# Optimization experiments

Measured on AMD Instinct MI355X. Metric: run time of the kernel, lower is better.

## Reference

```python
import jax, jax.numpy as jnp
import numpy as np

N_P, E_P = 150000, 1200000   # protein nodes / edges (512 complexes batched)
N_L, E_L = 16000, 64000      # ligand nodes / edges
E_I = 400000                 # interaction (distance) edges, bidirectional
B, D, L = 512, 64, 3         # graphs, hidden_dim_g, num_g_layers
ND, ED = 58, 6               # initial node / edge feature dims


def edge_softmax(logits, dst, n):
    # softmax over incoming edges of each destination node
    m = jax.ops.segment_max(logits, dst, num_segments=n)
    ex = jnp.exp(logits - m[dst])
    s = jax.ops.segment_sum(ex, dst, num_segments=n)
    return ex / (s[dst] + 1e-9)


def gcn_layer(h, src, dst, W, n):
    # GraphConvolution: sum-aggregate neighbors, linear, relu, residual
    agg = jax.ops.segment_sum(h[src], dst, num_segments=n)
    return jax.nn.relu(agg @ W) + h


def gat_layer(h, e, src, dst, Wh, We, a_s, a_d, a_e, n):
    # GraphAttention (edge-feature aware GAT): additive attention logits,
    # edge-softmax by destination, weighted message sum, relu, residual.
    x = h @ Wh                      # [N, D]
    ee = e @ We                     # [E, D]
    logit = jax.nn.leaky_relu(
        (x[src] * a_s).sum(-1) + (x[dst] * a_d).sum(-1) + (ee * a_e).sum(-1), 0.2)
    alpha = edge_softmax(logit, dst, n)
    out = jax.ops.segment_sum(alpha[:, None] * (x[src] + ee), dst, num_segments=n)
    return jax.nn.relu(out) + h


def setup_inputs() -> dict:
    key = jax.random.key(0)
    ks = jax.random.split(key, 40)
    p = lambda k, shape: jax.random.normal(k, shape, jnp.float32) * 0.05
    h_p = jax.random.normal(ks[0], (N_P, ND), jnp.float32)
    e_p = jax.random.normal(ks[1], (E_P, ED), jnp.float32)
    src_p = jax.random.randint(ks[2], (E_P,), 0, N_P, jnp.int32)
    dst_p = jax.random.randint(ks[3], (E_P,), 0, N_P, jnp.int32)
    h_l = jax.random.normal(ks[4], (N_L, ND), jnp.float32)
    e_l = jax.random.normal(ks[5], (E_L, ED), jnp.float32)
    src_l = jax.random.randint(ks[6], (E_L,), 0, N_L, jnp.int32)
    dst_l = jax.random.randint(ks[7], (E_L,), 0, N_L, jnp.int32)
    coordinate = jax.random.normal(ks[8], (N_P + N_L, 3), jnp.float32) * 10.0
    # interaction edges: protein <-> ligand (ligand nodes offset by N_P)
    sp = jax.random.randint(ks[9], (E_I // 2,), 0, N_P, jnp.int32)
    dl = jax.random.randint(ks[10], (E_I // 2,), N_P, N_P + N_L, jnp.int32)
    src_i = jnp.concatenate([sp, dl])
    dst_i = jnp.concatenate([dl, sp])
    # graph ids for batched readout (balanced partition, monotone)
    gid_p = jnp.asarray(np.arange(N_P) * B // N_P, jnp.int32)
    gid_l = jnp.asarray(np.arange(N_L) * B // N_L, jnp.int32)
    gid_j = jnp.concatenate([gid_p, gid_l])
    return {
        'h_p': h_p, 'e_p': e_p, 'src_p': src_p, 'dst_p': dst_p,
        'h_l': h_l, 'e_l': e_l, 'src_l': src_l, 'dst_l': dst_l,
        'coordinate': coordinate, 'src_i': src_i, 'dst_i': dst_i, 'gid_j': gid_j,
        'Wn_p': p(ks[11], (ND, D)), 'We_p': p(ks[12], (ED, D)),
        'Wn_l': p(ks[13], (ND, D)), 'We_l': p(ks[14], (ED, D)),
        'Wemb_in': p(ks[15], (D, D)), 'Wemb_ie': p(ks[16], (1, D)),
        'Wc': p(ks[17], (L, D, D)),
        'Al_h': p(ks[18], (L, D, D)), 'Al_e': p(ks[19], (L, D, D)),
        'al_s': p(ks[20], (L, D)), 'al_d': p(ks[21], (L, D)), 'al_e': p(ks[22], (L, D)),
        'Ai_h': p(ks[23], (L, D, D)), 'Ai_e': p(ks[24], (L, D, D)),
        'ai_s': p(ks[25], (L, D)), 'ai_d': p(ks[26], (L, D)), 'ai_e': p(ks[27], (L, D)),
        'W1': p(ks[28], (D, D)), 'W2': p(ks[29], (D, 1)),
    }


def reference(h_p, e_p, src_p, dst_p, h_l, e_l, src_l, dst_l, coordinate,
              src_i, dst_i, gid_j, Wn_p, We_p, Wn_l, We_l, Wemb_in, Wemb_ie,
              Wc, Al_h, Al_e, al_s, al_d, al_e, Ai_h, Ai_e, ai_s, ai_d, ai_e,
              W1, W2):
    # node / edge embeddings (bias-free linears)
    hp = h_p @ Wn_p
    ep = e_p @ We_p
    hl = h_l @ Wn_l
    el = e_l @ We_l
    n_p, n_l = hp.shape[0], hl.shape[0]
    # protein branch: GraphConvolution stack
    for i in range(Wc.shape[0]):
        hp = gcn_layer(hp, src_p, dst_p, Wc[i], n_p)
    # ligand branch: GraphAttention stack (bond edge features)
    for i in range(Al_h.shape[0]):
        hl = gat_layer(hl, el, src_l, dst_l, Al_h[i], Al_e[i],
                       al_s[i], al_d[i], al_e[i], n_l)
    # join graphs: node states concatenated, edge feature = pair distance
    hj = jnp.concatenate([hp, hl], axis=0) @ Wemb_in          # [N_P+N_L, D]
    dist = jnp.sqrt(((coordinate[src_i] - coordinate[dst_i]) ** 2)
                    .sum(-1, keepdims=True) + 1e-12)           # [E_I, 1]
    vdw = dist @ Wemb_ie                                       # [E_I, D]
    n_j = n_p + n_l
    for i in range(Ai_h.shape[0]):
        hj = gat_layer(hj, vdw, src_i, dst_i, Ai_h[i], Ai_e[i],
                       ai_s[i], ai_d[i], ai_e[i], n_j)
    # sum readout per complex, then 2-layer bias-free MLP
    readout = jax.ops.segment_sum(hj, gid_j, num_segments=B)   # [B, D]
    return jax.nn.relu(readout @ W1) @ W2                      # [B, 1]
```

## Files before the change

kernel.cpp:

```cpp
#include <hip/hip_runtime.h>
#include <math.h>

#define THREADS 256

#define N_P 150000
#define E_P 1200000
#define N_L 16000
#define E_L 64000
#define E_I 400000
#define N_J (N_P + N_L)
#define NB  512
#define DIM 64
#define NLAYER 3
#define SCAN_TILE 1024

typedef float f4 __attribute__((ext_vector_type(4)));

static __device__ __forceinline__ float wred_sum(float v) {
    #pragma unroll
    for (int o = 32; o; o >>= 1) v += __shfl_xor(v, o);
    return v;
}
static __device__ __forceinline__ float gred_max(float v) {
    #pragma unroll
    for (int o = 1; o <= 8; o <<= 1) v = fmaxf(v, __shfl_xor(v, o));
    return v;
}
static __device__ __forceinline__ float gred_sum(float v) {
    #pragma unroll
    for (int o = 1; o <= 8; o <<= 1) v += __shfl_xor(v, o);
    return v;
}

__global__ void hist_k(const int* __restrict__ dst, int* __restrict__ cnt,
                       int* __restrict__ slot, int E)
{
    int e = blockIdx.x * THREADS + threadIdx.x;
    if (e >= E) return;
    slot[e] = atomicAdd(&cnt[dst[e]], 1);
}

__global__ void scan_local(const int* __restrict__ in, int* __restrict__ out,
                           int* __restrict__ partials, int n)
{
    __shared__ int lds[256];
    int t = threadIdx.x;
    int base = blockIdx.x * SCAN_TILE + t * 4;
    int v0 = base + 0 < n ? in[base + 0] : 0;
    int v1 = base + 1 < n ? in[base + 1] : 0;
    int v2 = base + 2 < n ? in[base + 2] : 0;
    int v3 = base + 3 < n ? in[base + 3] : 0;
    int s = v0 + v1 + v2 + v3;
    lds[t] = s;
    __syncthreads();
    #pragma unroll
    for (int off = 1; off < 256; off <<= 1) {
        int x = (t >= off) ? lds[t - off] : 0;
        __syncthreads();
        lds[t] += x;
        __syncthreads();
    }
    int excl = lds[t] - s;
    if (base + 0 < n) out[base + 0] = excl;
    if (base + 1 < n) out[base + 1] = excl + v0;
    if (base + 2 < n) out[base + 2] = excl + v0 + v1;
    if (base + 3 < n) out[base + 3] = excl + v0 + v1 + v2;
    if (t == 255) partials[blockIdx.x] = lds[255];
}

__global__ void scan_part(int* __restrict__ partials, int np)
{
    __shared__ int lds[256];
    int t = threadIdx.x;
    int v = t < np ? partials[t] : 0;
    lds[t] = v;
    __syncthreads();
    #pragma unroll
    for (int off = 1; off < 256; off <<= 1) {
        int x = (t >= off) ? lds[t - off] : 0;
        __syncthreads();
        lds[t] += x;
        __syncthreads();
    }
    if (t < np) partials[t] = lds[t] - v;
}

__global__ void scan_add(int* __restrict__ out, const int* __restrict__ partials,
                         int n, int etotal)
{
    int i = blockIdx.x * THREADS + threadIdx.x;
    if (i < n) out[i] += partials[i / SCAN_TILE];
    if (i == 0) out[n] = etotal;
}

__global__ void fill_p_k(const int* __restrict__ src, const int* __restrict__ dst,
                         const int* __restrict__ slot, const int* __restrict__ rp,
                         int* __restrict__ esrc, int E)
{
    int e = blockIdx.x * THREADS + threadIdx.x;
    if (e >= E) return;
    esrc[rp[dst[e]] + slot[e]] = src[e];
}

__global__ void fill_l_k(const int* __restrict__ src, const int* __restrict__ dst,
                         const int* __restrict__ slot, const int* __restrict__ rp,
                         int* __restrict__ esrc, int* __restrict__ eid, int E)
{
    int e = blockIdx.x * THREADS + threadIdx.x;
    if (e >= E) return;
    int pos = rp[dst[e]] + slot[e];
    esrc[pos] = src[e];
    eid[pos] = e;
}

__global__ void fill_i_k(const int* __restrict__ src, const int* __restrict__ dst,
                         const int* __restrict__ slot, const int* __restrict__ rp,
                         const float* __restrict__ coord,
                         int* __restrict__ esrc, float* __restrict__ dsorted, int E)
{
    int e = blockIdx.x * THREADS + threadIdx.x;
    if (e >= E) return;
    int s = src[e], d = dst[e];
    int pos = rp[d] + slot[e];
    esrc[pos] = s;
    float dx = coord[s * 3 + 0] - coord[d * 3 + 0];
    float dy = coord[s * 3 + 1] - coord[d * 3 + 1];
    float dz = coord[s * 3 + 2] - coord[d * 3 + 2];
    dsorted[pos] = sqrtf(dx * dx + dy * dy + dz * dz + 1e-12f);
}

template<int K, int EPI>
__global__ __launch_bounds__(256, 8)
void gemm64_k(const float* __restrict__ X, const float* __restrict__ W,
              const float* __restrict__ RES, const float* __restrict__ a1,
              const float* __restrict__ a2, float* __restrict__ Y,
              float* __restrict__ S1, float* __restrict__ S2, int N)
{
    __shared__ float Xs[64][68];
    int t = threadIdx.x;
    int tx = t & 15, ty = t >> 4;
    int rbase = blockIdx.x * 64;
    if constexpr (K % 4 == 0) {
        #pragma unroll
        for (int j = t; j < 16 * K; j += 256) {
            int r = j / (K / 4), k4 = j % (K / 4);
            int row = rbase + r;
            f4 v = {0.f, 0.f, 0.f, 0.f};
            if (row < N) v = *(const f4*)&X[(long)row * K + k4 * 4];
            *(f4*)&Xs[r][k4 * 4] = v;
        }
    } else {
        for (int j = t; j < 64 * K; j += 256) {
            int r = j / K, k = j - r * K;
            int row = rbase + r;
            Xs[r][k] = (row < N) ? X[(long)row * K + k] : 0.f;
        }
    }
    __syncthreads();
    f4 acc[4] = {{0,0,0,0},{0,0,0,0},{0,0,0,0},{0,0,0,0}};
    #pragma unroll 4
    for (int k = 0; k < K; ++k) {
        f4 wv = *(const f4*)&W[k * DIM + tx * 4];
        #pragma unroll
        for (int i = 0; i < 4; ++i) {
            float xv = Xs[ty * 4 + i][k];
            acc[i] += wv * xv;
        }
    }
    #pragma unroll
    for (int i = 0; i < 4; ++i) {
        int row = rbase + ty * 4 + i;
        if (row >= N) continue;
        f4 y = acc[i];
        if constexpr (EPI == 1) {
            f4 res = *(const f4*)&RES[(long)row * DIM + tx * 4];
            #pragma unroll
            for (int c = 0; c < 4; ++c) y[c] = fmaxf(y[c], 0.f) + res[c];
        }
        *(f4*)&Y[(long)row * DIM + tx * 4] = y;
    }
    if constexpr (EPI == 2) {
        f4 a1v = *(const f4*)&a1[tx * 4];
        f4 a2v = *(const f4*)&a2[tx * 4];
        #pragma unroll
        for (int i = 0; i < 4; ++i) {
            float s = acc[i][0]*a1v[0] + acc[i][1]*a1v[1] + acc[i][2]*a1v[2] + acc[i][3]*a1v[3];
            float d = acc[i][0]*a2v[0] + acc[i][1]*a2v[1] + acc[i][2]*a2v[2] + acc[i][3]*a2v[3];
            #pragma unroll
            for (int o = 1; o <= 8; o <<= 1) {
                s += __shfl_xor(s, o);
                d += __shfl_xor(d, o);
            }
            int row = rbase + ty * 4 + i;
            if (tx == 0 && row < N) { S1[row] = s; S2[row] = d; }
        }
    }
    if constexpr (EPI == 3) {
        f4 a1v = *(const f4*)&a1[tx * 4];
        #pragma unroll
        for (int i = 0; i < 4; ++i) {
            float s = acc[i][0]*a1v[0] + acc[i][1]*a1v[1] + acc[i][2]*a1v[2] + acc[i][3]*a1v[3];
            #pragma unroll
            for (int o = 1; o <= 8; o <<= 1) s += __shfl_xor(s, o);
            int row = rbase + ty * 4 + i;
            if (tx == 0 && row < N) S1[row] = s;
        }
    }
}

template<int JOIN>
__global__ __launch_bounds__(256, 6)
void gcn_fused_k(const float* __restrict__ Hin, const int* __restrict__ rp,
                 const int* __restrict__ esrc, const float* __restrict__ W,
                 const float* __restrict__ W2, float* __restrict__ Hout, int N)
{
    __shared__ float Xs[32][68];
    __shared__ float Ws[64][64];
    int t = threadIdx.x;
    int gl = t & 15, g = t >> 4, wb = (t & 63) & 48;
    int rbase = blockIdx.x * 32;
    for (int i = t; i < 1024; i += 256)
        *(f4*)&Ws[(i * 4) >> 6][(i * 4) & 63] = *(const f4*)&W[i * 4];
    #pragma unroll
    for (int it = 0; it < 2; ++it) {
        int ln = it * 16 + g;
        int node = rbase + ln;
        f4 acc = {0.f, 0.f, 0.f, 0.f};
        if (node < N) {
            int lo = rp[node], hi = rp[node + 1];
            for (int cb = lo; cb < hi; cb += 16) {
                int cnt = min(16, hi - cb);
                int sidx = (gl < cnt) ? esrc[cb + gl] : 0;
                int p = 0;
                for (; p + 3 < cnt; p += 4) {
                    int s0 = __shfl(sidx, wb + p + 0);
                    int s1 = __shfl(sidx, wb + p + 1);
                    int s2 = __shfl(sidx, wb + p + 2);
                    int s3 = __shfl(sidx, wb + p + 3);
                    f4 v0 = *(const f4*)&Hin[(long)s0 * DIM + gl * 4];
                    f4 v1 = *(const f4*)&Hin[(long)s1 * DIM + gl * 4];
                    f4 v2 = *(const f4*)&Hin[(long)s2 * DIM + gl * 4];
                    f4 v3 = *(const f4*)&Hin[(long)s3 * DIM + gl * 4];
                    acc += v0; acc += v1; acc += v2; acc += v3;
                }
                for (; p < cnt; ++p) {
                    int s = __shfl(sidx, wb + p);
                    acc += *(const f4*)&Hin[(long)s * DIM + gl * 4];
                }
            }
        }
        *(f4*)&Xs[ln][gl * 4] = acc;
    }
    __syncthreads();
    int tx = t & 15, ty = t >> 4;
    f4 acc[2] = {{0,0,0,0},{0,0,0,0}};
    #pragma unroll 4
    for (int k = 0; k < DIM; ++k) {
        f4 wv = *(const f4*)&Ws[k][tx * 4];
        acc[0] += wv * Xs[ty * 2 + 0][k];
        acc[1] += wv * Xs[ty * 2 + 1][k];
    }
    f4 yv[2];
    #pragma unroll
    for (int i = 0; i < 2; ++i) {
        int row = rbase + ty * 2 + i;
        int rr = row < N ? row : 0;
        f4 res = *(const f4*)&Hin[(long)rr * DIM + tx * 4];
        #pragma unroll
        for (int c = 0; c < 4; ++c) yv[i][c] = fmaxf(acc[i][c], 0.f) + res[c];
    }
    if constexpr (!JOIN) {
        #pragma unroll
        for (int i = 0; i < 2; ++i) {
            int row = rbase + ty * 2 + i;
            if (row < N) *(f4*)&Hout[(long)row * DIM + tx * 4] = yv[i];
        }
    } else {
        __syncthreads();
        *(f4*)&Xs[ty * 2 + 0][tx * 4] = yv[0];
        *(f4*)&Xs[ty * 2 + 1][tx * 4] = yv[1];
        for (int i = t; i < 1024; i += 256)
            *(f4*)&Ws[(i * 4) >> 6][(i * 4) & 63] = *(const f4*)&W2[i * 4];
        __syncthreads();
        f4 a2[2] = {{0,0,0,0},{0,0,0,0}};
        #pragma unroll 4
        for (int k = 0; k < DIM; ++k) {
            f4 wv = *(const f4*)&Ws[k][tx * 4];
            a2[0] += wv * Xs[ty * 2 + 0][k];
            a2[1] += wv * Xs[ty * 2 + 1][k];
        }
        #pragma unroll
        for (int i = 0; i < 2; ++i) {
            int row = rbase + ty * 2 + i;
            if (row < N) *(f4*)&Hout[(long)row * DIM + tx * 4] = a2[i];
        }
    }
}

__global__ __launch_bounds__(256, 8)
void gat_l_k(const float* __restrict__ X, const float* __restrict__ Sn,
             const float* __restrict__ Dn, const float* __restrict__ Et,
             const float* __restrict__ EE, const int* __restrict__ rp,
             const int* __restrict__ esrc, const int* __restrict__ eid,
             float* __restrict__ H, int N)
{
    int t = threadIdx.x;
    int gl = t & 15, g = t >> 4, wb = (t & 63) & 48;
    int node = blockIdx.x * 16 + g;
    int lo = 0, hi = 0;
    float dn = 0.f;
    if (node < N) { lo = rp[node]; hi = rp[node + 1]; dn = Dn[node]; }
    float m = -INFINITY, ssum = 0.f;
    f4 msg = {0.f, 0.f, 0.f, 0.f};
    for (int cb = lo; cb < hi; cb += 16) {
        int cnt = min(16, hi - cb);
        int sidx = 0, eidx = 0;
        float l = -INFINITY;
        if (gl < cnt) {
            sidx = esrc[cb + gl];
            eidx = eid[cb + gl];
            l = Sn[sidx] + dn + Et[eidx];
            l = (l >= 0.f) ? l : 0.2f * l;
        }
        float mnew = fmaxf(m, gred_max(l));
        float scale = expf(m - mnew);
        float ex = (gl < cnt) ? expf(l - mnew) : 0.f;
        ssum = ssum * scale + gred_sum(ex);
        msg *= scale;
        int p = 0;
        for (; p + 1 < cnt; p += 2) {
            float e0 = __shfl(ex, wb + p + 0); int s0 = __shfl(sidx, wb + p + 0);
            int   q0 = __shfl(eidx, wb + p + 0);
            float e1 = __shfl(ex, wb + p + 1); int s1 = __shfl(sidx, wb + p + 1);
            int   q1 = __shfl(eidx, wb + p + 1);
            f4 x0 = *(const f4*)&X[(long)s0 * DIM + gl * 4];
            f4 f0 = *(const f4*)&EE[(long)q0 * DIM + gl * 4];
            f4 x1 = *(const f4*)&X[(long)s1 * DIM + gl * 4];
            f4 f1 = *(const f4*)&EE[(long)q1 * DIM + gl * 4];
            msg += (x0 + f0) * e0;
            msg += (x1 + f1) * e1;
        }
        for (; p < cnt; ++p) {
            float ep = __shfl(ex, wb + p);
            int s = __shfl(sidx, wb + p);
            int e = __shfl(eidx, wb + p);
            f4 xv = *(const f4*)&X[(long)s * DIM + gl * 4];
            f4 ev = *(const f4*)&EE[(long)e * DIM + gl * 4];
            msg += (xv + ev) * ep;
        }
        m = mnew;
    }
    float inv = 1.f / (ssum + 1e-9f);
    if (node < N) {
        long o = (long)node * DIM + gl * 4;
        f4 h = *(const f4*)&H[o];
        f4 r;
        #pragma unroll
        for (int c = 0; c < 4; ++c) r[c] = fmaxf(msg[c] * inv, 0.f) + h[c];
        *(f4*)&H[o] = r;
    }
}

__global__ __launch_bounds__(256, 8)
void gat_i_k(const float* __restrict__ X, const float* __restrict__ Sn,
             const float* __restrict__ Dn, const float* __restrict__ dsorted,
             const float* __restrict__ cbuf, const int* __restrict__ rp,
             const int* __restrict__ esrc, float* __restrict__ H, int N)
{
    int t = threadIdx.x;
    int gl = t & 15, g = t >> 4, wb = (t & 63) & 48;
    int node = blockIdx.x * 16 + g;
    float ce = cbuf[64];
    int lo = 0, hi = 0;
    float dn = 0.f;
    if (node < N) { lo = rp[node]; hi = rp[node + 1]; dn = Dn[node]; }
    float m = -INFINITY, ssum = 0.f, wl = 0.f;
    f4 msg = {0.f, 0.f, 0.f, 0.f};
    for (int cb = lo; cb < hi; cb += 16) {
        int cnt = min(16, hi - cb);
        int sidx = 0;
        float dv = 0.f, l = -INFINITY;
        if (gl < cnt) {
            sidx = esrc[cb + gl];
            dv = dsorted[cb + gl];
            l = Sn[sidx] + dn + dv * ce;
            l = (l >= 0.f) ? l : 0.2f * l;
        }
        float mnew = fmaxf(m, gred_max(l));
        float scale = expf(m - mnew);
        float ex = (gl < cnt) ? expf(l - mnew) : 0.f;
        ssum = ssum * scale + gred_sum(ex);
        wl = wl * scale + ex * dv;
        msg *= scale;
        int p = 0;
        for (; p + 3 < cnt; p += 4) {
            float e0 = __shfl(ex, wb + p + 0); int s0 = __shfl(sidx, wb + p + 0);
            float e1 = __shfl(ex, wb + p + 1); int s1 = __shfl(sidx, wb + p + 1);
            float e2 = __shfl(ex, wb + p + 2); int s2 = __shfl(sidx, wb + p + 2);
            float e3 = __shfl(ex, wb + p + 3); int s3 = __shfl(sidx, wb + p + 3);
            f4 v0 = *(const f4*)&X[(long)s0 * DIM + gl * 4];
            f4 v1 = *(const f4*)&X[(long)s1 * DIM + gl * 4];
            f4 v2 = *(const f4*)&X[(long)s2 * DIM + gl * 4];
            f4 v3 = *(const f4*)&X[(long)s3 * DIM + gl * 4];
            msg += v0 * e0; msg += v1 * e1; msg += v2 * e2; msg += v3 * e3;
        }
        for (; p < cnt; ++p) {
            float ep = __shfl(ex, wb + p);
            int s = __shfl(sidx, wb + p);
            msg += *(const f4*)&X[(long)s * DIM + gl * 4] * ep;
        }
        m = mnew;
    }
    float wsum = gred_sum(wl);
    float inv = 1.f / (ssum + 1e-9f);
    if (node < N) {
        long o = (long)node * DIM + gl * 4;
        f4 c4 = *(const f4*)&cbuf[gl * 4];
        f4 h = *(const f4*)&H[o];
        f4 r;
        #pragma unroll
        for (int c = 0; c < 4; ++c) {
            float v = (msg[c] + wsum * c4[c]) * inv;
            r[c] = fmaxf(v, 0.f) + h[c];
        }
        *(f4*)&H[o] = r;
    }
}

__global__ void cvec_all_k(const float* __restrict__ wie, const float* __restrict__ Ae,
                           const float* __restrict__ ae, float* __restrict__ cbuf)
{
    int L = blockIdx.x;
    int d = threadIdx.x;
    const float* A = Ae + (size_t)L * DIM * DIM;
    float c = 0.f;
    #pragma unroll
    for (int k = 0; k < DIM; ++k) c = fmaf(wie[k], A[k * DIM + d], c);
    cbuf[L * 80 + d] = c;
    float ce = wred_sum(c * ae[L * DIM + d]);
    if (d == 0) cbuf[L * 80 + 64] = ce;
}

__global__ __launch_bounds__(256, 1)
void readout_mlp_k(const float* __restrict__ HJ, const float* __restrict__ W1,
                   const float* __restrict__ W2, float* __restrict__ out)
{
    __shared__ float part[4][DIM];
    int t = threadIdx.x, wv = t >> 6, lane = t & 63;
    int b = blockIdx.x;
    float r = 0.f;
    long s0 = ((long)b * N_P + NB - 1) / NB;
    long e0 = ((long)(b + 1) * N_P + NB - 1) / NB;
    for (long n = s0 + wv; n < e0; n += 4) r += HJ[n * DIM + lane];
    long s1 = ((long)b * N_L + NB - 1) / NB;
    long e1 = ((long)(b + 1) * N_L + NB - 1) / NB;
    for (long n = s1 + wv; n < e1; n += 4) r += HJ[(N_P + n) * DIM + lane];
    part[wv][lane] = r;
    __syncthreads();
    if (wv != 0) return;
    r = part[0][lane] + part[1][lane] + part[2][lane] + part[3][lane];
    float acc = 0.f;
    #pragma unroll
    for (int k = 0; k < DIM; ++k) acc = fmaf(__shfl(r, k), W1[k * DIM + lane], acc);
    acc = fmaxf(acc, 0.f) * W2[lane];
    acc = wred_sum(acc);
    if (lane == 0) out[b] = acc;
}

extern "C" void kernel_launch(void* const* d_in, const int* in_sizes, int n_in,
                              void* d_out, int out_size, void* d_ws, size_t ws_size,
                              hipStream_t stream) {
    const float* h_p    = (const float*)d_in[0];
    const int*   src_p  = (const int*)d_in[2];
    const int*   dst_p  = (const int*)d_in[3];
    const float* h_l    = (const float*)d_in[4];
    const float* e_l    = (const float*)d_in[5];
    const int*   src_l  = (const int*)d_in[6];
    const int*   dst_l  = (const int*)d_in[7];
    const float* coord  = (const float*)d_in[8];
    const int*   src_i  = (const int*)d_in[9];
    const int*   dst_i  = (const int*)d_in[10];
    const float* Wn_p   = (const float*)d_in[12];
    const float* Wn_l   = (const float*)d_in[14];
    const float* We_l   = (const float*)d_in[15];
    const float* Wemb_in= (const float*)d_in[16];
    const float* Wemb_ie= (const float*)d_in[17];
    const float* Wc     = (const float*)d_in[18];
    const float* Al_h   = (const float*)d_in[19];
    const float* Al_e   = (const float*)d_in[20];
    const float* al_s   = (const float*)d_in[21];
    const float* al_d   = (const float*)d_in[22];
    const float* al_e   = (const float*)d_in[23];
    const float* Ai_h   = (const float*)d_in[24];
    const float* Ai_e   = (const float*)d_in[25];
    const float* ai_s   = (const float*)d_in[26];
    const float* ai_d   = (const float*)d_in[27];
    const float* ai_e   = (const float*)d_in[28];
    const float* W1     = (const float*)d_in[29];
    const float* W2     = (const float*)d_in[30];
    float* out = (float*)d_out;

    char* ws = (char*)d_ws;
    auto alloc = [&](size_t bytes) -> void* {
        char* p = ws;
        ws += (bytes + 255) & ~(size_t)255;
        return (void*)p;
    };
    float* HP    = (float*)alloc((size_t)N_P * DIM * 4);
    float* HL    = (float*)alloc((size_t)N_L * DIM * 4);
    float* EL    = (float*)alloc((size_t)E_L * DIM * 4);
    float* EE    = (float*)alloc((size_t)E_L * DIM * 4);
    float* HJ    = (float*)alloc((size_t)N_J * DIM * 4);
    float* XJ    = (float*)alloc((size_t)N_J * DIM * 4);
    float* SN    = (float*)alloc((size_t)N_J * 4);
    float* DN    = (float*)alloc((size_t)N_J * 4);
    float* ET    = (float*)alloc((size_t)E_L * 4);
    int*   cnt_p = (int*)alloc((size_t)N_P * 4);
    int*   cnt_l = (int*)alloc((size_t)N_L * 4);
    int*   cnt_i = (int*)alloc((size_t)N_J * 4);
    int*   rp_p  = (int*)alloc((size_t)(N_P + 1) * 4);
    int*   rp_l  = (int*)alloc((size_t)(N_L + 1) * 4);
    int*   rp_i  = (int*)alloc((size_t)(N_J + 1) * 4);
    int*   slot  = (int*)alloc((size_t)E_P * 4);
    int*   esrc_p= (int*)alloc((size_t)E_P * 4);
    int*   esrc_l= (int*)alloc((size_t)E_L * 4);
    int*   eid_l = (int*)alloc((size_t)E_L * 4);
    int*   esrc_i= (int*)alloc((size_t)E_I * 4);
    float* dsort = (float*)alloc((size_t)E_I * 4);
    int*   parts = (int*)alloc(256 * 4);
    float* CBUF  = (float*)alloc(3 * 80 * 4);
    (void)ws_size; (void)in_sizes; (void)n_in; (void)out_size;

    auto cdiv = [](int a, int b) { return (a + b - 1) / b; };

    hipMemsetAsync(cnt_p, 0, (size_t)N_P * 4, stream);
    hipMemsetAsync(cnt_l, 0, (size_t)N_L * 4, stream);
    hipMemsetAsync(cnt_i, 0, (size_t)N_J * 4, stream);
    auto build = [&](const int* dst, int* cnt, int* rp, int E, int N) {
        hist_k<<<cdiv(E, THREADS), THREADS, 0, stream>>>(dst, cnt, slot, E);
        int nb = cdiv(N, SCAN_TILE);
        scan_local<<<nb, 256, 0, stream>>>(cnt, rp, parts, N);
        scan_part<<<1, 256, 0, stream>>>(parts, nb);
        scan_add<<<cdiv(N, THREADS), THREADS, 0, stream>>>(rp, parts, N, E);
    };
    build(dst_p, cnt_p, rp_p, E_P, N_P);
    fill_p_k<<<cdiv(E_P, THREADS), THREADS, 0, stream>>>(src_p, dst_p, slot, rp_p, esrc_p, E_P);
    build(dst_l, cnt_l, rp_l, E_L, N_L);
    fill_l_k<<<cdiv(E_L, THREADS), THREADS, 0, stream>>>(src_l, dst_l, slot, rp_l, esrc_l, eid_l, E_L);
    build(dst_i, cnt_i, rp_i, E_I, N_J);
    fill_i_k<<<cdiv(E_I, THREADS), THREADS, 0, stream>>>(src_i, dst_i, slot, rp_i, coord, esrc_i, dsort, E_I);

    cvec_all_k<<<3, 64, 0, stream>>>(Wemb_ie, Ai_e, ai_e, CBUF);

    gemm64_k<58, 0><<<cdiv(N_P, 64), THREADS, 0, stream>>>(h_p, Wn_p, nullptr, nullptr, nullptr,
                                                           HP, nullptr, nullptr, N_P);
    gemm64_k<58, 0><<<cdiv(N_L, 64), THREADS, 0, stream>>>(h_l, Wn_l, nullptr, nullptr, nullptr,
                                                           HL, nullptr, nullptr, N_L);
    gemm64_k<6, 0><<<cdiv(E_L, 64), THREADS, 0, stream>>>(e_l, We_l, nullptr, nullptr, nullptr,
                                                          EL, nullptr, nullptr, E_L);

    for (int i = 0; i < NLAYER; ++i) {
        const float* Wh = Al_h + (size_t)i * DIM * DIM;
        const float* We = Al_e + (size_t)i * DIM * DIM;
        gemm64_k<64, 2><<<cdiv(N_L, 64), THREADS, 0, stream>>>(HL, Wh, nullptr,
                                                               al_s + i * DIM, al_d + i * DIM,
                                                               XJ, SN, DN, N_L);
        gemm64_k<64, 3><<<cdiv(E_L, 64), THREADS, 0, stream>>>(EL, We, nullptr,
                                                               al_e + i * DIM, nullptr,
                                                               EE, ET, nullptr, E_L);
        gat_l_k<<<cdiv(N_L, 16), THREADS, 0, stream>>>(XJ, SN, DN, ET, EE, rp_l, esrc_l,
                                                       eid_l, HL, N_L);
    }

    gcn_fused_k<0><<<cdiv(N_P, 32), THREADS, 0, stream>>>(HP, rp_p, esrc_p,
                                                          Wc + 0 * DIM * DIM, nullptr, XJ, N_P);
    gcn_fused_k<0><<<cdiv(N_P, 32), THREADS, 0, stream>>>(XJ, rp_p, esrc_p,
                                                          Wc + 1 * (size_t)DIM * DIM, nullptr, HP, N_P);
    gcn_fused_k<1><<<cdiv(N_P, 32), THREADS, 0, stream>>>(HP, rp_p, esrc_p,
                                                          Wc + 2 * (size_t)DIM * DIM, Wemb_in, HJ, N_P);

    gemm64_k<64, 0><<<cdiv(N_L, 64), THREADS, 0, stream>>>(HL, Wemb_in, nullptr, nullptr, nullptr,
                                                           HJ + (size_t)N_P * DIM, nullptr, nullptr, N_L);

    for (int i = 0; i < NLAYER; ++i) {
        const float* Wh = Ai_h + (size_t)i * DIM * DIM;
        gemm64_k<64, 2><<<cdiv(N_J, 64), THREADS, 0, stream>>>(HJ, Wh, nullptr,
                                                               ai_s + i * DIM, ai_d + i * DIM,
                                                               XJ, SN, DN, N_J);
        gat_i_k<<<cdiv(N_J, 16), THREADS, 0, stream>>>(XJ, SN, DN, dsort, CBUF + i * 80, rp_i,
                                                       esrc_i, HJ, N_J);
    }

    readout_mlp_k<<<NB, THREADS, 0, stream>>>(HJ, W1, W2, out);
}
```

Baseline: 742.2 us.

## Fuse interaction GAT projection into aggregation via aggregate-then-transform reordering

Each interaction GAT layer used to run a separate GEMM producing X = H·Wh plus attention scalars, then a gather kernel over X. Attention scalars are now computed from H directly using precomputed Wh·a_s and Wh·a_d vectors, H is aggregated with softmax weights, and the aggregate is multiplied by Wh inside the same kernel. The next layer's scalars come from the epilogue, and the GCN and ligand embedding kernels emit the first layer's scalars. This drops three GEMM launches and their N×64 intermediate round trips, at the cost of ping-pong buffers and lower occupancy in the fused kernel.

Result: faster. 688.6 us (-7.2%).

```diff
diff --git a/kernel.cpp b/kernel.cpp
--- a/kernel.cpp
+++ b/kernel.cpp
@@ -31,6 +31,12 @@
     for (int o = 1; o <= 8; o <<= 1) v += __shfl_xor(v, o);
     return v;
 }
+static __device__ __forceinline__ float gdot16(f4 y, f4 a) {
+    float s = y[0]*a[0] + y[1]*a[1] + y[2]*a[2] + y[3]*a[3];
+    #pragma unroll
+    for (int o = 1; o <= 8; o <<= 1) s += __shfl_xor(s, o);
+    return s;
+}
 
 __global__ void hist_k(const int* __restrict__ dst, int* __restrict__ cnt,
                        int* __restrict__ slot, int E)
@@ -212,7 +218,9 @@
 __global__ __launch_bounds__(256, 6)
 void gcn_fused_k(const float* __restrict__ Hin, const int* __restrict__ rp,
                  const int* __restrict__ esrc, const float* __restrict__ W,
-                 const float* __restrict__ W2, float* __restrict__ Hout, int N)
+                 const float* __restrict__ W2, const float* __restrict__ ash,
+                 const float* __restrict__ adh, float* __restrict__ Hout,
+                 float* __restrict__ SnO, float* __restrict__ DnO, int N)
 {
     __shared__ float Xs[32][68];
     __shared__ float Ws[64][64];
@@ -294,6 +302,126 @@
             int row = rbase + ty * 2 + i;
             if (row < N) *(f4*)&Hout[(long)row * DIM + tx * 4] = a2[i];
         }
+        f4 av = *(const f4*)&ash[tx * 4];
+        f4 bv = *(const f4*)&adh[tx * 4];
+        float s0 = gdot16(a2[0], av);
+        float d0 = gdot16(a2[0], bv);
+        float s1 = gdot16(a2[1], av);
+        float d1 = gdot16(a2[1], bv);
+        if (tx == 0) {
+            int row0 = rbase + ty * 2, row1 = row0 + 1;
+            if (row0 < N) { SnO[row0] = s0; DnO[row0] = d0; }
+            if (row1 < N) { SnO[row1] = s1; DnO[row1] = d1; }
+        }
+    }
+}
+
+template<int LAST>
+__global__ __launch_bounds__(256, 6)
+void gat_i_fused_k(const float* __restrict__ Hin, const float* __restrict__ Sn,
+                   const float* __restrict__ Dn, const float* __restrict__ dsorted,
+                   const float* __restrict__ pb, const float* __restrict__ pbn,
+                   const float* __restrict__ Wh, const int* __restrict__ rp,
+                   const int* __restrict__ esrc, float* __restrict__ Hout,
+                   float* __restrict__ SnO, float* __restrict__ DnO, int N)
+{
+    __shared__ float Xs[32][68];
+    __shared__ float Ws[64][64];
+    __shared__ float wlS[32];
+    __shared__ float invS[32];
+    int t = threadIdx.x;
+    int gl = t & 15, g = t >> 4, wb = (t & 63) & 48;
+    int rbase = blockIdx.x * 32;
+    float ce = pb[64];
+    for (int i = t; i < 1024; i += 256)
+        *(f4*)&Ws[(i * 4) >> 6][(i * 4) & 63] = *(const f4*)&Wh[i * 4];
+    #pragma unroll
+    for (int it = 0; it < 2; ++it) {
+        int ln = it * 16 + g;
+        int node = rbase + ln;
+        int lo = 0, hi = 0;
+        float dn = 0.f;
+        if (node < N) { lo = rp[node]; hi = rp[node + 1]; dn = Dn[node]; }
+        float m = -INFINITY, ssum = 0.f, wl = 0.f;
+        f4 agg = {0.f, 0.f, 0.f, 0.f};
+        for (int cb = lo; cb < hi; cb += 16) {
+            int cnt = min(16, hi - cb);
+            int sidx = 0;
+            float dv = 0.f, l = -INFINITY;
+            if (gl < cnt) {
+                sidx = esrc[cb + gl];
+                dv = dsorted[cb + gl];
+                l = Sn[sidx] + dn + dv * ce;
+                l = (l >= 0.f) ? l : 0.2f * l;
+            }
+            float mnew = fmaxf(m, gred_max(l));
+            float scale = expf(m - mnew);
+            float ex = (gl < cnt) ? expf(l - mnew) : 0.f;
+            ssum = ssum * scale + gred_sum(ex);
+            wl = wl * scale + ex * dv;
+            agg *= scale;
+            int p = 0;
+            for (; p + 3 < cnt; p += 4) {
+                float e0 = __shfl(ex, wb + p + 0); int s0 = __shfl(sidx, wb + p + 0);
+                float e1 = __shfl(ex, wb + p + 1); int s1 = __shfl(sidx, wb + p + 1);
+                float e2 = __shfl(ex, wb + p + 2); int s2 = __shfl(sidx, wb + p + 2);
+                float e3 = __shfl(ex, wb + p + 3); int s3 = __shfl(sidx, wb + p + 3);
+                f4 v0 = *(const f4*)&Hin[(long)s0 * DIM + gl * 4];
+                f4 v1 = *(const f4*)&Hin[(long)s1 * DIM + gl * 4];
+                f4 v2 = *(const f4*)&Hin[(long)s2 * DIM + gl * 4];
+                f4 v3 = *(const f4*)&Hin[(long)s3 * DIM + gl * 4];
+                agg += v0 * e0; agg += v1 * e1; agg += v2 * e2; agg += v3 * e3;
+            }
+            for (; p < cnt; ++p) {
+                float ep = __shfl(ex, wb + p);
+                int s = __shfl(sidx, wb + p);
+                agg += *(const f4*)&Hin[(long)s * DIM + gl * 4] * ep;
+            }
+            m = mnew;
+        }
+        float wsum = gred_sum(wl);
+        *(f4*)&Xs[ln][gl * 4] = agg;
+        if (gl == 0) {
+            wlS[ln] = wsum;
+            invS[ln] = 1.f / (ssum + 1e-9f);
+        }
+    }
+    __syncthreads();
+    int tx = t & 15, ty = t >> 4;
+    f4 acc0 = {0,0,0,0}, acc1 = {0,0,0,0};
+    #pragma unroll 4
+    for (int k = 0; k < DIM; ++k) {
+        f4 wv = *(const f4*)&Ws[k][tx * 4];
+        acc0 += wv * Xs[ty * 2 + 0][k];
+        acc1 += wv * Xs[ty * 2 + 1][k];
+    }
+    int r0 = ty * 2, r1 = r0 + 1;
+    int row0 = rbase + r0, row1 = rbase + r1;
+    f4 c4 = *(const f4*)&pb[tx * 4];
+    float wl0 = wlS[r0], wl1 = wlS[r1];
+    float i0 = invS[r0], i1 = invS[r1];
+    int rr0 = row0 < N ? row0 : 0, rr1 = row1 < N ? row1 : 0;
+    f4 h0 = *(const f4*)&Hin[(long)rr0 * DIM + tx * 4];
+    f4 h1 = *(const f4*)&Hin[(long)rr1 * DIM + tx * 4];
+    f4 y0, y1;
+    #pragma unroll
+    for (int c = 0; c < 4; ++c) {
+        y0[c] = fmaxf((acc0[c] + wl0 * c4[c]) * i0, 0.f) + h0[c];
+        y1[c] = fmaxf((acc1[c] + wl1 * c4[c]) * i1, 0.f) + h1[c];
+    }
+    if (row0 < N) *(f4*)&Hout[(long)row0 * DIM + tx * 4] = y0;
+    if (row1 < N) *(f4*)&Hout[(long)row1 * DIM + tx * 4] = y1;
+    if constexpr (!LAST) {
+        f4 av = *(const f4*)&pbn[80 + tx * 4];
+        f4 bv = *(const f4*)&pbn[144 + tx * 4];
+        float s0 = gdot16(y0, av);
+        float d0 = gdot16(y0, bv);
+        float s1 = gdot16(y1, av);
+        float d1 = gdot16(y1, bv);
+        if (tx == 0) {
+            if (row0 < N) { SnO[row0] = s0; DnO[row0] = d0; }
+            if (row1 < N) { SnO[row1] = s1; DnO[row1] = d1; }
+        }
     }
 }
 
@@ -361,84 +489,30 @@
     }
 }
 
-__global__ __launch_bounds__(256, 8)
-void gat_i_k(const float* __restrict__ X, const float* __restrict__ Sn,
-             const float* __restrict__ Dn, const float* __restrict__ dsorted,
-             const float* __restrict__ cbuf, const int* __restrict__ rp,
-             const int* __restrict__ esrc, float* __restrict__ H, int N)
-{
-    int t = threadIdx.x;
-    int gl = t & 15, g = t >> 4, wb = (t & 63) & 48;
-    int node = blockIdx.x * 16 + g;
-    float ce = cbuf[64];
-    int lo = 0, hi = 0;
-    float dn = 0.f;
-    if (node < N) { lo = rp[node]; hi = rp[node + 1]; dn = Dn[node]; }
-    float m = -INFINITY, ssum = 0.f, wl = 0.f;
-    f4 msg = {0.f, 0.f, 0.f, 0.f};
-    for (int cb = lo; cb < hi; cb += 16) {
-        int cnt = min(16, hi - cb);
-        int sidx = 0;
-        float dv = 0.f, l = -INFINITY;
-        if (gl < cnt) {
-            sidx = esrc[cb + gl];
-            dv = dsorted[cb + gl];
-            l = Sn[sidx] + dn + dv * ce;
-            l = (l >= 0.f) ? l : 0.2f * l;
-        }
-        float mnew = fmaxf(m, gred_max(l));
-        float scale = expf(m - mnew);
-        float ex = (gl < cnt) ? expf(l - mnew) : 0.f;
-        ssum = ssum * scale + gred_sum(ex);
-        wl = wl * scale + ex * dv;
-        msg *= scale;
-        int p = 0;
-        for (; p + 3 < cnt; p += 4) {
-            float e0 = __shfl(ex, wb + p + 0); int s0 = __shfl(sidx, wb + p + 0);
-            float e1 = __shfl(ex, wb + p + 1); int s1 = __shfl(sidx, wb + p + 1);
-            float e2 = __shfl(ex, wb + p + 2); int s2 = __shfl(sidx, wb + p + 2);
-            float e3 = __shfl(ex, wb + p + 3); int s3 = __shfl(sidx, wb + p + 3);
-            f4 v0 = *(const f4*)&X[(long)s0 * DIM + gl * 4];
-            f4 v1 = *(const f4*)&X[(long)s1 * DIM + gl * 4];
-            f4 v2 = *(const f4*)&X[(long)s2 * DIM + gl * 4];
-            f4 v3 = *(const f4*)&X[(long)s3 * DIM + gl * 4];
-            msg += v0 * e0; msg += v1 * e1; msg += v2 * e2; msg += v3 * e3;
-        }
-        for (; p < cnt; ++p) {
-            float ep = __shfl(ex, wb + p);
-            int s = __shfl(sidx, wb + p);
-            msg += *(const f4*)&X[(long)s * DIM + gl * 4] * ep;
-        }
-        m = mnew;
-    }
-    float wsum = gred_sum(wl);
-    float inv = 1.f / (ssum + 1e-9f);
-    if (node < N) {
-        long o = (long)node * DIM + gl * 4;
-        f4 c4 = *(const f4*)&cbuf[gl * 4];
-        f4 h = *(const f4*)&H[o];
-        f4 r;
-        #pragma unroll
-        for (int c = 0; c < 4; ++c) {
-            float v = (msg[c] + wsum * c4[c]) * inv;
-            r[c] = fmaxf(v, 0.f) + h[c];
-        }
-        *(f4*)&H[o] = r;
-    }
-}
-
 __global__ void cvec_all_k(const float* __restrict__ wie, const float* __restrict__ Ae,
-                           const float* __restrict__ ae, float* __restrict__ cbuf)
+                           const float* __restrict__ Ah, const float* __restrict__ ae,
+                           const float* __restrict__ as_, const float* __restrict__ ad_,
+                           float* __restrict__ pbuf)
 {
     int L = blockIdx.x;
     int d = threadIdx.x;
-    const float* A = Ae + (size_t)L * DIM * DIM;
+    const float* Aev = Ae + (size_t)L * DIM * DIM;
+    const float* Ahv = Ah + (size_t)L * DIM * DIM;
     float c = 0.f;
     #pragma unroll
-    for (int k = 0; k < DIM; ++k) c = fmaf(wie[k], A[k * DIM + d], c);
-    cbuf[L * 80 + d] = c;
+    for (int k = 0; k < DIM; ++k) c = fmaf(wie[k], Aev[k * DIM + d], c);
+    pbuf[L * 256 + d] = c;
     float ce = wred_sum(c * ae[L * DIM + d]);
-    if (d == 0) cbuf[L * 80 + 64] = ce;
+    if (d == 0) pbuf[L * 256 + 64] = ce;
+    float s = 0.f, dd = 0.f;
+    #pragma unroll
+    for (int j = 0; j < DIM; ++j) {
+        float w = Ahv[d * DIM + j];
+        s = fmaf(w, as_[L * DIM + j], s);
+        dd = fmaf(w, ad_[L * DIM + j], dd);
+    }
+    pbuf[L * 256 + 80 + d] = s;
+    pbuf[L * 256 + 144 + d] = dd;
 }
 
 __global__ __launch_bounds__(256, 1)
@@ -512,8 +586,10 @@
     float* EE    = (float*)alloc((size_t)E_L * DIM * 4);
     float* HJ    = (float*)alloc((size_t)N_J * DIM * 4);
     float* XJ    = (float*)alloc((size_t)N_J * DIM * 4);
-    float* SN    = (float*)alloc((size_t)N_J * 4);
-    float* DN    = (float*)alloc((size_t)N_J * 4);
+    float* SNa   = (float*)alloc((size_t)N_J * 4);
+    float* DNa   = (float*)alloc((size_t)N_J * 4);
+    float* SNb   = (float*)alloc((size_t)N_J * 4);
+    float* DNb   = (float*)alloc((size_t)N_J * 4);
     float* ET    = (float*)alloc((size_t)E_L * 4);
     int*   cnt_p = (int*)alloc((size_t)N_P * 4);
     int*   cnt_l = (int*)alloc((size_t)N_L * 4);
@@ -528,7 +604,7 @@
     int*   esrc_i= (int*)alloc((size_t)E_I * 4);
     float* dsort = (float*)alloc((size_t)E_I * 4);
     int*   parts = (int*)alloc(256 * 4);
-    float* CBUF  = (float*)alloc(3 * 80 * 4);
+    float* PBUF  = (float*)alloc(3 * 256 * 4);
     (void)ws_size; (void)in_sizes; (void)n_in; (void)out_size;
 
     auto cdiv = [](int a, int b) { return (a + b - 1) / b; };
@@ -550,7 +626,7 @@
     build(dst_i, cnt_i, rp_i, E_I, N_J);
     fill_i_k<<<cdiv(E_I, THREADS), THREADS, 0, stream>>>(src_i, dst_i, slot, rp_i, coord, esrc_i, dsort, E_I);
 
-    cvec_all_k<<<3, 64, 0, stream>>>(Wemb_ie, Ai_e, ai_e, CBUF);
+    cvec_all_k<<<3, 64, 0, stream>>>(Wemb_ie, Ai_e, Ai_h, ai_e, ai_s, ai_d, PBUF);
 
     gemm64_k<58, 0><<<cdiv(N_P, 64), THREADS, 0, stream>>>(h_p, Wn_p, nullptr, nullptr, nullptr,
                                                            HP, nullptr, nullptr, N_P);
@@ -564,32 +640,44 @@
         const float* We = Al_e + (size_t)i * DIM * DIM;
         gemm64_k<64, 2><<<cdiv(N_L, 64), THREADS, 0, stream>>>(HL, Wh, nullptr,
                                                                al_s + i * DIM, al_d + i * DIM,
-                                                               XJ, SN, DN, N_L);
+                                                               XJ, SNa, DNa, N_L);
         gemm64_k<64, 3><<<cdiv(E_L, 64), THREADS, 0, stream>>>(EL, We, nullptr,
                                                                al_e + i * DIM, nullptr,
                                                                EE, ET, nullptr, E_L);
-        gat_l_k<<<cdiv(N_L, 16), THREADS, 0, stream>>>(XJ, SN, DN, ET, EE, rp_l, esrc_l,
+        gat_l_k<<<cdiv(N_L, 16), THREADS, 0, stream>>>(XJ, SNa, DNa, ET, EE, rp_l, esrc_l,
                                                        eid_l, HL, N_L);
     }
 
     gcn_fused_k<0><<<cdiv(N_P, 32), THREADS, 0, stream>>>(HP, rp_p, esrc_p,
-                                                          Wc + 0 * DIM * DIM, nullptr, XJ, N_P);
+                                                          Wc + 0 * DIM * DIM, nullptr,
+                                                          nullptr, nullptr, XJ,
+                                                          nullptr, nullptr, N_P);
     gcn_fused_k<0><<<cdiv(N_P, 32), THREADS, 0, stream>>>(XJ, rp_p, esrc_p,
-                                                          Wc + 1 * (size_t)DIM * DIM, nullptr, HP, N_P);
+                                                          Wc + 1 * (size_t)DIM * DIM, nullptr,
+                                                          nullptr, nullptr, HP,
+                                                          nullptr, nullptr, N_P);
     gcn_fused_k<1><<<cdiv(N_P, 32), THREADS, 0, stream>>>(HP, rp_p, esrc_p,
-                                                          Wc + 2 * (size_t)DIM * DIM, Wemb_in, HJ, N_P);
-
-    gemm64_k<64, 0><<<cdiv(N_L, 64), THREADS, 0, stream>>>(HL, Wemb_in, nullptr, nullptr, nullptr,
-                                                           HJ + (size_t)N_P * DIM, nullptr, nullptr, N_L);
-
-    for (int i = 0; i < NLAYER; ++i) {
-        const float* Wh = Ai_h + (size_t)i * DIM * DIM;
-        gemm64_k<64, 2><<<cdiv(N_J, 64), THREADS, 0, stream>>>(HJ, Wh, nullptr,
-                                                               ai_s + i * DIM, ai_d + i * DIM,
-                                                               XJ, SN, DN, N_J);
-        gat_i_k<<<cdiv(N_J, 16), THREADS, 0, stream>>>(XJ, SN, DN, dsort, CBUF + i * 80, rp_i,
-                                                       esrc_i, HJ, N_J);
-    }
-
-    readout_mlp_k<<<NB, THREADS, 0, stream>>>(HJ, W1, W2, out);
-}
+                                                          Wc + 2 * (size_t)DIM * DIM, Wemb_in,
+                                                          PBUF + 80, PBUF + 144, HJ,
+                                                          SNa, DNa, N_P);
+
+    gemm64_k<64, 2><<<cdiv(N_L, 64), THREADS, 0, stream>>>(HL, Wemb_in, nullptr,
+                                                           PBUF + 80, PBUF + 144,
+                                                           HJ + (size_t)N_P * DIM,
+                                                           SNa + N_P, DNa + N_P, N_L);
+
+    gat_i_fused_k<0><<<cdiv(N_J, 32), THREADS, 0, stream>>>(HJ, SNa, DNa, dsort,
+                                                            PBUF + 0, PBUF + 256,
+                                                            Ai_h + 0, rp_i, esrc_i,
+                                                            XJ, SNb, DNb, N_J);
+    gat_i_fused_k<0><<<cdiv(N_J, 32), THREADS, 0, stream>>>(XJ, SNb, DNb, dsort,
+                                                            PBUF + 256, PBUF + 512,
+                                                            Ai_h + 4096, rp_i, esrc_i,
+                                                            HJ, SNa, DNa, N_J);
+    gat_i_fused_k<1><<<cdiv(N_J, 32), THREADS, 0, stream>>>(HJ, SNa, DNa, dsort,
+                                                            PBUF + 512, PBUF + 512,
+                                                            Ai_h + 8192, rp_i, esrc_i,
+                                                            XJ, nullptr, nullptr, N_J);
+
+    readout_mlp_k<<<NB, THREADS, 0, stream>>>(XJ, W1, W2, out);
+}
```
